# Optimization experiments

Hardware: AMD Instinct MI355X
Metric: run time of the kernel (lower is better)

Reference implementation:

```python
import jax, jax.numpy as jnp
import numpy as np

N, C_IN, C_OUT, J = 4096, 256, 256, 2
ATT_SLICE = C_OUT * J  # 512
DENSITY = 0.01
NEG_FILL = -1e20


def _sparse_lap(key, n):
    k1, k2 = jax.random.split(key)
    vals = jax.random.normal(k1, (n, n), dtype=jnp.float32)
    mask = jax.random.uniform(k2, (n, n)) < DENSITY
    return vals * mask + jnp.eye(n, dtype=jnp.float32)


def setup_inputs() -> dict:
    key = jax.random.key(0)
    ks = jax.random.split(key, 12)
    s = 0.05
    return {
        "x": jax.random.normal(ks[0], (N, C_IN), dtype=jnp.float32),
        "Lup": _sparse_lap(ks[1], N),
        "Ld": _sparse_lap(ks[2], N),
        "P": _sparse_lap(ks[3], N),
        "Wirr_w": jax.random.normal(ks[4], (J, C_OUT, C_IN), dtype=jnp.float32) * s,
        "Wirr_b": jax.random.normal(ks[5], (J, C_OUT), dtype=jnp.float32) * s,
        "Wsol_w": jax.random.normal(ks[6], (J, C_OUT, C_IN), dtype=jnp.float32) * s,
        "Wsol_b": jax.random.normal(ks[7], (J, C_OUT), dtype=jnp.float32) * s,
        "Whar_w": jax.random.normal(ks[8], (C_OUT, C_IN), dtype=jnp.float32) * s,
        "Whar_b": jax.random.normal(ks[9], (C_OUT,), dtype=jnp.float32) * s,
        "att_irr": jax.random.normal(ks[10], (2 * ATT_SLICE, 1), dtype=jnp.float32) * s,
        "att_sol": jax.random.normal(ks[11], (2 * ATT_SLICE, 1), dtype=jnp.float32) * s,
    }


def _branch(x, L, Ww, Wb, att):
    # x_cat = concat_j(Linear_j(x)) : [N, J*C_OUT]
    x_cat = (jnp.einsum('nc,jdc->njd', x, Ww) + Wb).reshape(x.shape[0], -1)
    src = x_cat @ att[:ATT_SLICE, :]   # [N,1]
    dst = x_cat @ att[ATT_SLICE:, :]   # [N,1]
    E = jax.nn.leaky_relu(src + dst.T, negative_slope=0.01)  # [N,N]
    E = jnp.where(L != 0, E, NEG_FILL)
    alpha = jax.nn.softmax(E, axis=-1)
    z = (alpha @ x) @ Ww[0].T + Wb[0]
    for p in range(1, J):  # Laplacian-power diffusion
        alpha = alpha @ L
        z = z + (alpha @ x) @ Ww[p].T + Wb[p]
    return z


def reference(x, Lup, Ld, P, Wirr_w, Wirr_b, Wsol_w, Wsol_b, Whar_w, Whar_b, att_irr, att_sol):
    z_i = _branch(x, Ld, Wirr_w, Wirr_b, att_irr)
    z_s = _branch(x, Lup, Wsol_w, Wsol_b, att_sol)
    z_har = (P @ x) @ Whar_w.T + Whar_b
    return z_i + z_s + z_har
```

## Files before the change

kernel.cpp:

```cpp
#include <hip/hip_runtime.h>

#define NROW 4096
#define CH   256
#define MAXNNZ 128

typedef short  short8  __attribute__((ext_vector_type(8)));
typedef unsigned short ushort8 __attribute__((ext_vector_type(8)));
typedef float  f32x4   __attribute__((ext_vector_type(4)));

__device__ inline unsigned short f2bf(float f) {
  unsigned u = __float_as_uint(f);
  return (unsigned short)((u + 0x7fffu + ((u >> 16) & 1u)) >> 16);
}
__device__ inline float bf2f(unsigned short h) {
  return __uint_as_float((unsigned)h << 16);
}
__device__ inline int mbcnt64(unsigned long long m, int base) {
  int t = __builtin_amdgcn_mbcnt_lo((unsigned)m, (unsigned)base);
  return __builtin_amdgcn_mbcnt_hi((unsigned)(m >> 32), t);
}

__global__ __launch_bounds__(256, 4) void build_csr3(
    const float* __restrict__ L0, const float* __restrict__ L1,
    const float* __restrict__ L2, int* __restrict__ idx,
    float* __restrict__ val, int* __restrict__ cnt) {
  __shared__ int   sj[4][MAXNNZ];
  __shared__ float sv[4][MAXNNZ];
  const int mat = blockIdx.y;
  const float* L = (mat == 0) ? L0 : (mat == 1) ? L1 : L2;
  const int wi = threadIdx.x >> 6, lane = threadIdx.x & 63;
  const int row = blockIdx.x * 4 + wi;
  const float4* Lrow = (const float4*)(L + (size_t)row * NROW);

  float4 v0  = Lrow[lane],        v1  = Lrow[64 + lane];
  float4 v2  = Lrow[128 + lane],  v3  = Lrow[192 + lane];
  float4 v4  = Lrow[256 + lane],  v5  = Lrow[320 + lane];
  float4 v6  = Lrow[384 + lane],  v7  = Lrow[448 + lane];
  float4 v8  = Lrow[512 + lane],  v9  = Lrow[576 + lane];
  float4 v10 = Lrow[640 + lane],  v11 = Lrow[704 + lane];
  float4 v12 = Lrow[768 + lane],  v13 = Lrow[832 + lane];
  float4 v14 = Lrow[896 + lane],  v15 = Lrow[960 + lane];
  __builtin_amdgcn_sched_barrier(0);

  int base = 0;
#define PROCQ(q, cb) {                                                         \
    bool a0 = q.x != 0.f, a1 = q.y != 0.f, a2 = q.z != 0.f, a3 = q.w != 0.f;   \
    unsigned long long b0 = __ballot(a0), b1 = __ballot(a1);                   \
    unsigned long long b2 = __ballot(a2), b3 = __ballot(a3);                   \
    int off = mbcnt64(b3, mbcnt64(b2, mbcnt64(b1, mbcnt64(b0, base))));        \
    if (a0) { if (off < MAXNNZ) { sj[wi][off] = (cb);     sv[wi][off] = q.x; } ++off; } \
    if (a1) { if (off < MAXNNZ) { sj[wi][off] = (cb) + 1; sv[wi][off] = q.y; } ++off; } \
    if (a2) { if (off < MAXNNZ) { sj[wi][off] = (cb) + 2; sv[wi][off] = q.z; } ++off; } \
    if (a3) { if (off < MAXNNZ) { sj[wi][off] = (cb) + 3; sv[wi][off] = q.w; } ++off; } \
    base += __popcll(b0) + __popcll(b1) + __popcll(b2) + __popcll(b3); }
  int cb = lane * 4;
  PROCQ(v0,  cb)        PROCQ(v1,  cb + 256)  PROCQ(v2,  cb + 512)  PROCQ(v3,  cb + 768)
  PROCQ(v4,  cb + 1024) PROCQ(v5,  cb + 1280) PROCQ(v6,  cb + 1536) PROCQ(v7,  cb + 1792)
  PROCQ(v8,  cb + 2048) PROCQ(v9,  cb + 2304) PROCQ(v10, cb + 2560) PROCQ(v11, cb + 2816)
  PROCQ(v12, cb + 3072) PROCQ(v13, cb + 3328) PROCQ(v14, cb + 3584) PROCQ(v15, cb + 3840)
#undef PROCQ

  size_t rbase = ((size_t)mat * NROW + row) * MAXNNZ;
  int2   ji = ((const int2*)sj[wi])[lane];
  float2 vf = ((const float2*)sv[wi])[lane];
  ((int2*)(idx + rbase))[lane] = ji;
  ((float2*)(val + rbase))[lane] = vf;
  if (lane == 0) cnt[mat * NROW + row] = base < MAXNNZ ? base : MAXNNZ;
}

__global__ void cvt_all(const float* __restrict__ x, const float* __restrict__ Wi,
                        const float* __restrict__ Ws, const float* __restrict__ Wh,
                        unsigned short* __restrict__ xbf, unsigned short* __restrict__ Bbf) {
  int i = blockIdx.x * 256 + threadIdx.x;
  const float* src; unsigned short* dst; int o;
  if (i < 262144)        { src = x;  dst = xbf;          o = i; }
  else if (i < 294912)   { src = Wi; dst = Bbf;          o = i - 262144; }
  else if (i < 327680)   { src = Ws; dst = Bbf + 131072; o = i - 294912; }
  else                   { src = Wh; dst = Bbf + 262144; o = i - 327680; }
  float4 v = ((const float4*)src)[o];
  ushort4 u;
  u.x = f2bf(v.x); u.y = f2bf(v.y); u.z = f2bf(v.z); u.w = f2bf(v.w);
  ((ushort4*)dst)[o] = u;
}

__global__ __launch_bounds__(256, 2) void gemm_mfma(const unsigned short* __restrict__ A,
                                                    const unsigned short* __restrict__ Bt,
                                                    unsigned short* __restrict__ Y) {
  __shared__ unsigned short sA[64 * 256];
  __shared__ unsigned short sB[64 * 256];
  const int m0 = blockIdx.x * 64, n0 = blockIdx.y * 64;
  const int tid = threadIdx.x, wid = tid >> 6, lane = tid & 63;

  for (int c = 0; c < 8; ++c) {
    int chunk = c * 256 + tid;
    int r  = chunk >> 5;
    int cb = (chunk & 31) * 16;
    int cbs = cb ^ ((r & 7) << 4);
    ushort8 va = *(const ushort8*)((const char*)(A  + (size_t)(m0 + r) * 256) + cb);
    *(ushort8*)((char*)sA + r * 512 + cbs) = va;
    ushort8 vb = *(const ushort8*)((const char*)(Bt + (size_t)(n0 + r) * 256) + cb);
    *(ushort8*)((char*)sB + r * 512 + cbs) = vb;
  }
  __syncthreads();

  const int wr = wid >> 1, wc = wid & 1;
  const int lr = lane & 15, kg = lane >> 4;
  f32x4 acc[2][2] = {};
#pragma unroll
  for (int ks = 0; ks < 8; ++ks) {
    int kb = ks * 64 + kg * 16;
    short8 a0, a1, b0, b1;
    { int r = wr * 32 + lr;      a0 = *(const short8*)((const char*)sA + r * 512 + (kb ^ ((r & 7) << 4))); }
    { int r = wr * 32 + 16 + lr; a1 = *(const short8*)((const char*)sA + r * 512 + (kb ^ ((r & 7) << 4))); }
    { int r = wc * 32 + lr;      b0 = *(const short8*)((const char*)sB + r * 512 + (kb ^ ((r & 7) << 4))); }
    { int r = wc * 32 + 16 + lr; b1 = *(const short8*)((const char*)sB + r * 512 + (kb ^ ((r & 7) << 4))); }
    acc[0][0] = __builtin_amdgcn_mfma_f32_16x16x32_bf16(a0, b0, acc[0][0], 0, 0, 0);
    acc[0][1] = __builtin_amdgcn_mfma_f32_16x16x32_bf16(a0, b1, acc[0][1], 0, 0, 0);
    acc[1][0] = __builtin_amdgcn_mfma_f32_16x16x32_bf16(a1, b0, acc[1][0], 0, 0, 0);
    acc[1][1] = __builtin_amdgcn_mfma_f32_16x16x32_bf16(a1, b1, acc[1][1], 0, 0, 0);
  }

#pragma unroll
  for (int mi = 0; mi < 2; ++mi)
#pragma unroll
    for (int ni = 0; ni < 2; ++ni) {
      int col = n0 + wc * 32 + ni * 16 + lr;
#pragma unroll
      for (int r4 = 0; r4 < 4; ++r4) {
        int row = m0 + wr * 32 + mi * 16 + kg * 4 + r4;
        Y[(size_t)row * 1280 + col] = f2bf(acc[mi][ni][r4]);
      }
    }
}

__global__ __launch_bounds__(256) void sdv_from_y(
    const unsigned short* __restrict__ Y, const float* __restrict__ ai,
    const float* __restrict__ as_, const float* __restrict__ bi,
    const float* __restrict__ bs, float* __restrict__ sdv) {
  __shared__ float satt[2048];
  __shared__ float sbias[4];
  int t = threadIdx.x, wi = t >> 6, lane = t & 63;
  for (int k = t; k < 1024; k += 256) { satt[k] = ai[k]; satt[1024 + k] = as_[k]; }
  {
    const float* av = (wi & 2) ? as_ : ai;
    const float* bv = (wi & 2) ? bs : bi;
    int off = (wi & 1) * 512;
    float b = 0.f;
    for (int k = lane; k < 512; k += 64) b += av[off + k] * bv[k];
    for (int o = 32; o; o >>= 1) b += __shfl_xor(b, o);
    if (lane == 0) sbias[wi] = b;
  }
  __syncthreads();

  int row = blockIdx.x * 4 + wi;
  const ushort8* yr = (const ushort8*)(Y + (size_t)row * 1280);
  ushort8 ya = yr[lane * 2], yb = yr[lane * 2 + 1];
  int c0 = lane * 16;
  int off = (lane < 32) ? 0 : 512;
  float a0 = 0.f, a1 = 0.f;
#pragma unroll
  for (int j = 0; j < 8; ++j) {
    float y = bf2f(ya[j]); int c = c0 + j;
    a0 += satt[off + c] * y; a1 += satt[off + 512 + c] * y;
  }
#pragma unroll
  for (int j = 0; j < 8; ++j) {
    float y = bf2f(yb[j]); int c = c0 + 8 + j;
    a0 += satt[off + c] * y; a1 += satt[off + 512 + c] * y;
  }
  for (int o = 16; o; o >>= 1) { a0 += __shfl_xor(a0, o); a1 += __shfl_xor(a1, o); }
  if (lane == 0)  { sdv[row] = a0 + sbias[0];            sdv[NROW + row] = a1 + sbias[1]; }
  if (lane == 32) { sdv[2 * NROW + row] = a0 + sbias[2]; sdv[3 * NROW + row] = a1 + sbias[3]; }
}

__global__ __launch_bounds__(256) void spmm_add(const int* __restrict__ idx,
                                                const float* __restrict__ val,
                                                const int* __restrict__ cnt,
                                                unsigned short* __restrict__ Y) {
  int br = blockIdx.y, row = blockIdx.x;
  int t = threadIdx.x, w = t >> 6, l = t & 63;
  __shared__ int   sj[MAXNNZ];
  __shared__ float sv[MAXNNZ];
  __shared__ float part[4][256];
  size_t rbase = ((size_t)br * NROW + row) * MAXNNZ;
  int n = cnt[br * NROW + row];
  if (t < n) { sj[t] = idx[rbase + t]; sv[t] = val[rbase + t]; }
  __syncthreads();
  int cs = br ? 768 : 256, cd = br ? 512 : 0;
  float4 acc = {0.f, 0.f, 0.f, 0.f};
  for (int k = w; k < n; k += 4) {
    ushort4 y = *(const ushort4*)(Y + (size_t)sj[k] * 1280 + cs + 4 * l);
    float a = sv[k];
    acc.x += a * bf2f(y.x); acc.y += a * bf2f(y.y);
    acc.z += a * bf2f(y.z); acc.w += a * bf2f(y.w);
  }
  ((float4*)part[w])[l] = acc;
  __syncthreads();
  if (t < 64) {
    unsigned short* yp = Y + (size_t)row * 1280 + cd + 4 * t;
    ushort4 yb = *(const ushort4*)yp;
    ushort4 o;
    o.x = f2bf(bf2f(yb.x) + part[0][4 * t]     + part[1][4 * t]     + part[2][4 * t]     + part[3][4 * t]);
    o.y = f2bf(bf2f(yb.y) + part[0][4 * t + 1] + part[1][4 * t + 1] + part[2][4 * t + 1] + part[3][4 * t + 1]);
    o.z = f2bf(bf2f(yb.z) + part[0][4 * t + 2] + part[1][4 * t + 2] + part[2][4 * t + 2] + part[3][4 * t + 2]);
    o.w = f2bf(bf2f(yb.w) + part[0][4 * t + 3] + part[1][4 * t + 3] + part[2][4 * t + 3] + part[3][4 * t + 3]);
    *(ushort4*)yp = o;
  }
}

__global__ __launch_bounds__(256) void final_z(const int* __restrict__ idx,
                        const float* __restrict__ val, const int* __restrict__ cnt,
                        const float* __restrict__ sdv,
                        const unsigned short* __restrict__ Y,
                        const float* __restrict__ bi, const float* __restrict__ bs,
                        const float* __restrict__ bh, float* __restrict__ Z) {
  int row = blockIdx.x, t = threadIdx.x, w = t >> 6, l = t & 63;
  __shared__ float sa[MAXNNZ];
  __shared__ int   sj[MAXNNZ];
  __shared__ float red[4];
  __shared__ float part[4][256];
  float4 acc = {0.f, 0.f, 0.f, 0.f};

  for (int br = 0; br < 2; ++br) {
    size_t rbase = ((size_t)br * NROW + row) * MAXNNZ;
    int n = cnt[br * NROW + row];
    const float* srcv = sdv + (2 * br) * NROW;
    const float* dstv = sdv + (2 * br + 1) * NROW;
    float e = -1e30f;
    if (t < n) {
      int j = idx[rbase + t];
      sj[t] = j;
      float v = srcv[row] + dstv[j];
      e = v >= 0.f ? v : 0.01f * v;
    }
    float m = e;
    for (int o = 32; o; o >>= 1) m = fmaxf(m, __shfl_xor(m, o));
    if ((t & 63) == 0) red[t >> 6] = m;
    __syncthreads();
    m = fmaxf(fmaxf(red[0], red[1]), fmaxf(red[2], red[3]));
    __syncthreads();
    float p = (t < n) ? expf(e - m) : 0.f;
    float s = p;
    for (int o = 32; o; o >>= 1) s += __shfl_xor(s, o);
    if ((t & 63) == 0) red[t >> 6] = s;
    __syncthreads();
    s = red[0] + red[1] + red[2] + red[3];
    if (t < n) sa[t] = p / s;
    __syncthreads();
    int cd = br ? 512 : 0;
    for (int k = w; k < n; k += 4) {
      ushort4 y = *(const ushort4*)(Y + (size_t)sj[k] * 1280 + cd + 4 * l);
      float a = sa[k];
      acc.x += a * bf2f(y.x); acc.y += a * bf2f(y.y);
      acc.z += a * bf2f(y.z); acc.w += a * bf2f(y.w);
    }
    __syncthreads();
  }

  {
    size_t rbase = ((size_t)2 * NROW + row) * MAXNNZ;
    int n = cnt[2 * NROW + row];
    if (t < n) { sj[t] = idx[rbase + t]; sa[t] = val[rbase + t]; }
    __syncthreads();
    for (int k = w; k < n; k += 4) {
      ushort4 y = *(const ushort4*)(Y + (size_t)sj[k] * 1280 + 1024 + 4 * l);
      float a = sa[k];
      acc.x += a * bf2f(y.x); acc.y += a * bf2f(y.y);
      acc.z += a * bf2f(y.z); acc.w += a * bf2f(y.w);
    }
  }
  ((float4*)part[w])[l] = acc;
  __syncthreads();
  if (t < 64) {
    float4 r;
    int c = 4 * t;
    r.x = part[0][c]     + part[1][c]     + part[2][c]     + part[3][c]     + bi[c]     + bi[256 + c]     + bs[c]     + bs[256 + c]     + bh[c];
    r.y = part[0][c + 1] + part[1][c + 1] + part[2][c + 1] + part[3][c + 1] + bi[c + 1] + bi[257 + c]     + bs[c + 1] + bs[257 + c]     + bh[c + 1];
    r.z = part[0][c + 2] + part[1][c + 2] + part[2][c + 2] + part[3][c + 2] + bi[c + 2] + bi[258 + c]     + bs[c + 2] + bs[258 + c]     + bh[c + 2];
    r.w = part[0][c + 3] + part[1][c + 3] + part[2][c + 3] + part[3][c + 3] + bi[c + 3] + bi[259 + c]     + bs[c + 3] + bs[259 + c]     + bh[c + 3];
    *(float4*)(Z + (size_t)row * 256 + c) = r;
  }
}

extern "C" void kernel_launch(void* const* d_in, const int* in_sizes, int n_in,
                              void* d_out, int out_size, void* d_ws, size_t ws_size,
                              hipStream_t stream) {
  const float* x      = (const float*)d_in[0];
  const float* Lup    = (const float*)d_in[1];
  const float* Ld     = (const float*)d_in[2];
  const float* P      = (const float*)d_in[3];
  const float* Wirr_w = (const float*)d_in[4];
  const float* Wirr_b = (const float*)d_in[5];
  const float* Wsol_w = (const float*)d_in[6];
  const float* Wsol_b = (const float*)d_in[7];
  const float* Whar_w = (const float*)d_in[8];
  const float* Whar_b = (const float*)d_in[9];
  const float* att_i  = (const float*)d_in[10];
  const float* att_s  = (const float*)d_in[11];
  float* Z = (float*)d_out;

  char* w = (char*)d_ws;
  auto alloc = [&](size_t bytes) { void* p = (void*)w; w += (bytes + 255) & ~(size_t)255; return p; };

  int*   idx  = (int*)alloc((size_t)3 * NROW * MAXNNZ * 4);
  float* val  = (float*)alloc((size_t)3 * NROW * MAXNNZ * 4);
  int*   cnt  = (int*)alloc((size_t)3 * NROW * 4);
  float* sdv  = (float*)alloc(4 * NROW * 4);
  unsigned short* xbf = (unsigned short*)alloc((size_t)NROW * CH * 2);
  unsigned short* Bbf = (unsigned short*)alloc((size_t)1280 * CH * 2);
  unsigned short* Y   = (unsigned short*)alloc((size_t)NROW * 1280 * 2);

  build_csr3<<<dim3(NROW / 4, 3), 256, 0, stream>>>(Ld, Lup, P, idx, val, cnt);

  cvt_all<<<(262144 + 32768 + 32768 + 16384) / 256, 256, 0, stream>>>(x, Wirr_w, Wsol_w, Whar_w, xbf, Bbf);

  gemm_mfma<<<dim3(NROW / 64, 1280 / 64), 256, 0, stream>>>(xbf, Bbf, Y);

  sdv_from_y<<<NROW / 4, 256, 0, stream>>>(Y, att_i, att_s, Wirr_b, Wsol_b, sdv);

  spmm_add<<<dim3(NROW, 2), 256, 0, stream>>>(idx, val, cnt, Y);

  final_z<<<NROW, 256, 0, stream>>>(idx, val, cnt, sdv, Y, Wirr_b, Wsol_b, Whar_b, Z);
}
```

Measured before the change: 114.1 us.

## Fuse CSR scan with GEMM via interleaved blocks and merge sdv into spmm

The dense-to-CSR scan and the MFMA projection GEMM now run in one launch. Every tenth block does a GEMM tile in two K-halves with a smaller shared buffer, and the rest scan one row each, split across four waves. The separate sdv and spmm kernels are merged into a single per-row kernel that computes both attention dot products and both branch SpMMs. The aim is fewer launches and letting the GEMM work overlap the bandwidth-bound scan of the three dense matrices. In exchange the scan now uses one block per row instead of four rows per block, and the merged row kernel adds extra barriers and shared memory.

Measured after the change: 107.8 us. 1.06x faster.

```diff
diff --git a/kernel.cpp b/kernel.cpp
--- a/kernel.cpp
+++ b/kernel.cpp
@@ -18,54 +18,6 @@
 __device__ inline int mbcnt64(unsigned long long m, int base) {
   int t = __builtin_amdgcn_mbcnt_lo((unsigned)m, (unsigned)base);
   return __builtin_amdgcn_mbcnt_hi((unsigned)(m >> 32), t);
-}
-
-__global__ __launch_bounds__(256, 4) void build_csr3(
-    const float* __restrict__ L0, const float* __restrict__ L1,
-    const float* __restrict__ L2, int* __restrict__ idx,
-    float* __restrict__ val, int* __restrict__ cnt) {
-  __shared__ int   sj[4][MAXNNZ];
-  __shared__ float sv[4][MAXNNZ];
-  const int mat = blockIdx.y;
-  const float* L = (mat == 0) ? L0 : (mat == 1) ? L1 : L2;
-  const int wi = threadIdx.x >> 6, lane = threadIdx.x & 63;
-  const int row = blockIdx.x * 4 + wi;
-  const float4* Lrow = (const float4*)(L + (size_t)row * NROW);
-
-  float4 v0  = Lrow[lane],        v1  = Lrow[64 + lane];
-  float4 v2  = Lrow[128 + lane],  v3  = Lrow[192 + lane];
-  float4 v4  = Lrow[256 + lane],  v5  = Lrow[320 + lane];
-  float4 v6  = Lrow[384 + lane],  v7  = Lrow[448 + lane];
-  float4 v8  = Lrow[512 + lane],  v9  = Lrow[576 + lane];
-  float4 v10 = Lrow[640 + lane],  v11 = Lrow[704 + lane];
-  float4 v12 = Lrow[768 + lane],  v13 = Lrow[832 + lane];
-  float4 v14 = Lrow[896 + lane],  v15 = Lrow[960 + lane];
-  __builtin_amdgcn_sched_barrier(0);
-
-  int base = 0;
-#define PROCQ(q, cb) {                                                         \
-    bool a0 = q.x != 0.f, a1 = q.y != 0.f, a2 = q.z != 0.f, a3 = q.w != 0.f;   \
-    unsigned long long b0 = __ballot(a0), b1 = __ballot(a1);                   \
-    unsigned long long b2 = __ballot(a2), b3 = __ballot(a3);                   \
-    int off = mbcnt64(b3, mbcnt64(b2, mbcnt64(b1, mbcnt64(b0, base))));        \
-    if (a0) { if (off < MAXNNZ) { sj[wi][off] = (cb);     sv[wi][off] = q.x; } ++off; } \
-    if (a1) { if (off < MAXNNZ) { sj[wi][off] = (cb) + 1; sv[wi][off] = q.y; } ++off; } \
-    if (a2) { if (off < MAXNNZ) { sj[wi][off] = (cb) + 2; sv[wi][off] = q.z; } ++off; } \
-    if (a3) { if (off < MAXNNZ) { sj[wi][off] = (cb) + 3; sv[wi][off] = q.w; } ++off; } \
-    base += __popcll(b0) + __popcll(b1) + __popcll(b2) + __popcll(b3); }
-  int cb = lane * 4;
-  PROCQ(v0,  cb)        PROCQ(v1,  cb + 256)  PROCQ(v2,  cb + 512)  PROCQ(v3,  cb + 768)
-  PROCQ(v4,  cb + 1024) PROCQ(v5,  cb + 1280) PROCQ(v6,  cb + 1536) PROCQ(v7,  cb + 1792)
-  PROCQ(v8,  cb + 2048) PROCQ(v9,  cb + 2304) PROCQ(v10, cb + 2560) PROCQ(v11, cb + 2816)
-  PROCQ(v12, cb + 3072) PROCQ(v13, cb + 3328) PROCQ(v14, cb + 3584) PROCQ(v15, cb + 3840)
-#undef PROCQ
-
-  size_t rbase = ((size_t)mat * NROW + row) * MAXNNZ;
-  int2   ji = ((const int2*)sj[wi])[lane];
-  float2 vf = ((const float2*)sv[wi])[lane];
-  ((int2*)(idx + rbase))[lane] = ji;
-  ((float2*)(val + rbase))[lane] = vf;
-  if (lane == 0) cnt[mat * NROW + row] = base < MAXNNZ ? base : MAXNNZ;
 }
 
 __global__ void cvt_all(const float* __restrict__ x, const float* __restrict__ Wi,
@@ -83,121 +35,188 @@
   ((ushort4*)dst)[o] = u;
 }
 
-__global__ __launch_bounds__(256, 2) void gemm_mfma(const unsigned short* __restrict__ A,
-                                                    const unsigned short* __restrict__ Bt,
-                                                    unsigned short* __restrict__ Y) {
-  __shared__ unsigned short sA[64 * 256];
-  __shared__ unsigned short sB[64 * 256];
-  const int m0 = blockIdx.x * 64, n0 = blockIdx.y * 64;
-  const int tid = threadIdx.x, wid = tid >> 6, lane = tid & 63;
-
-  for (int c = 0; c < 8; ++c) {
-    int chunk = c * 256 + tid;
-    int r  = chunk >> 5;
-    int cb = (chunk & 31) * 16;
-    int cbs = cb ^ ((r & 7) << 4);
-    ushort8 va = *(const ushort8*)((const char*)(A  + (size_t)(m0 + r) * 256) + cb);
-    *(ushort8*)((char*)sA + r * 512 + cbs) = va;
-    ushort8 vb = *(const ushort8*)((const char*)(Bt + (size_t)(n0 + r) * 256) + cb);
-    *(ushort8*)((char*)sB + r * 512 + cbs) = vb;
-  }
-  __syncthreads();
-
-  const int wr = wid >> 1, wc = wid & 1;
-  const int lr = lane & 15, kg = lane >> 4;
-  f32x4 acc[2][2] = {};
-#pragma unroll
-  for (int ks = 0; ks < 8; ++ks) {
-    int kb = ks * 64 + kg * 16;
-    short8 a0, a1, b0, b1;
-    { int r = wr * 32 + lr;      a0 = *(const short8*)((const char*)sA + r * 512 + (kb ^ ((r & 7) << 4))); }
-    { int r = wr * 32 + 16 + lr; a1 = *(const short8*)((const char*)sA + r * 512 + (kb ^ ((r & 7) << 4))); }
-    { int r = wc * 32 + lr;      b0 = *(const short8*)((const char*)sB + r * 512 + (kb ^ ((r & 7) << 4))); }
-    { int r = wc * 32 + 16 + lr; b1 = *(const short8*)((const char*)sB + r * 512 + (kb ^ ((r & 7) << 4))); }
-    acc[0][0] = __builtin_amdgcn_mfma_f32_16x16x32_bf16(a0, b0, acc[0][0], 0, 0, 0);
-    acc[0][1] = __builtin_amdgcn_mfma_f32_16x16x32_bf16(a0, b1, acc[0][1], 0, 0, 0);
-    acc[1][0] = __builtin_amdgcn_mfma_f32_16x16x32_bf16(a1, b0, acc[1][0], 0, 0, 0);
-    acc[1][1] = __builtin_amdgcn_mfma_f32_16x16x32_bf16(a1, b1, acc[1][1], 0, 0, 0);
-  }
-
-#pragma unroll
-  for (int mi = 0; mi < 2; ++mi)
-#pragma unroll
-    for (int ni = 0; ni < 2; ++ni) {
-      int col = n0 + wc * 32 + ni * 16 + lr;
-#pragma unroll
-      for (int r4 = 0; r4 < 4; ++r4) {
-        int row = m0 + wr * 32 + mi * 16 + kg * 4 + r4;
-        Y[(size_t)row * 1280 + col] = f2bf(acc[mi][ni][r4]);
+__global__ __launch_bounds__(256) void scan_gemm(
+    const float* __restrict__ L0, const float* __restrict__ L1,
+    const float* __restrict__ L2, int* __restrict__ idx,
+    float* __restrict__ val, int* __restrict__ cnt,
+    const unsigned short* __restrict__ A, const unsigned short* __restrict__ Bt,
+    unsigned short* __restrict__ Y) {
+  __shared__ __align__(16) union {
+    struct { unsigned short sA[64 * 128]; unsigned short sB[64 * 128]; } g;
+    struct { int sj[4][MAXNNZ]; float sv[4][MAXNNZ]; int scnt[4]; } c;
+  } u;
+  const int bid = blockIdx.x, tid = threadIdx.x;
+  const bool is_gemm = (bid < 12800) && (bid % 10 == 9);
+
+  if (is_gemm) {
+    const int gid = bid / 10;
+    const int m0 = (gid & 63) * 64, n0 = (gid >> 6) * 64;
+    const int wid = tid >> 6, lane = tid & 63;
+    const int wr = wid >> 1, wc = wid & 1, lr = lane & 15, kg = lane >> 4;
+    f32x4 acc[2][2] = {};
+#pragma unroll
+    for (int kh = 0; kh < 2; ++kh) {
+      for (int c = 0; c < 4; ++c) {
+        int chunk = c * 256 + tid;
+        int r  = chunk >> 4;
+        int cb = (chunk & 15) * 16;
+        int cbs = cb ^ ((r & 7) << 4);
+        ushort8 va = *(const ushort8*)((const char*)A  + (size_t)(m0 + r) * 512 + kh * 256 + cb);
+        *(ushort8*)((char*)u.g.sA + r * 256 + cbs) = va;
+        ushort8 vb = *(const ushort8*)((const char*)Bt + (size_t)(n0 + r) * 512 + kh * 256 + cb);
+        *(ushort8*)((char*)u.g.sB + r * 256 + cbs) = vb;
       }
-    }
-}
-
-__global__ __launch_bounds__(256) void sdv_from_y(
-    const unsigned short* __restrict__ Y, const float* __restrict__ ai,
+      __syncthreads();
+#pragma unroll
+      for (int ks = 0; ks < 4; ++ks) {
+        int kb = ks * 64 + kg * 16;
+        short8 a0, a1, b0, b1;
+        { int r = wr * 32 + lr;      a0 = *(const short8*)((const char*)u.g.sA + r * 256 + (kb ^ ((r & 7) << 4))); }
+        { int r = wr * 32 + 16 + lr; a1 = *(const short8*)((const char*)u.g.sA + r * 256 + (kb ^ ((r & 7) << 4))); }
+        { int r = wc * 32 + lr;      b0 = *(const short8*)((const char*)u.g.sB + r * 256 + (kb ^ ((r & 7) << 4))); }
+        { int r = wc * 32 + 16 + lr; b1 = *(const short8*)((const char*)u.g.sB + r * 256 + (kb ^ ((r & 7) << 4))); }
+        acc[0][0] = __builtin_amdgcn_mfma_f32_16x16x32_bf16(a0, b0, acc[0][0], 0, 0, 0);
+        acc[0][1] = __builtin_amdgcn_mfma_f32_16x16x32_bf16(a0, b1, acc[0][1], 0, 0, 0);
+        acc[1][0] = __builtin_amdgcn_mfma_f32_16x16x32_bf16(a1, b0, acc[1][0], 0, 0, 0);
+        acc[1][1] = __builtin_amdgcn_mfma_f32_16x16x32_bf16(a1, b1, acc[1][1], 0, 0, 0);
+      }
+      __syncthreads();
+    }
+#pragma unroll
+    for (int mi = 0; mi < 2; ++mi)
+#pragma unroll
+      for (int ni = 0; ni < 2; ++ni) {
+        int col = n0 + wc * 32 + ni * 16 + lr;
+#pragma unroll
+        for (int r4 = 0; r4 < 4; ++r4) {
+          int row = m0 + wr * 32 + mi * 16 + kg * 4 + r4;
+          Y[(size_t)row * 1280 + col] = f2bf(acc[mi][ni][r4]);
+        }
+      }
+  } else {
+    const int cid = bid - ((bid < 12800) ? (bid + 1) / 10 : 1280);
+    const int mat = cid >> 12, row = cid & 4095;
+    const float* L = (mat == 0) ? L0 : (mat == 1) ? L1 : L2;
+    const int wi = tid >> 6, lane = tid & 63;
+    const float4* Lseg = (const float4*)(L + (size_t)row * NROW) + wi * 256;
+
+    float4 v0 = Lseg[lane], v1 = Lseg[64 + lane], v2 = Lseg[128 + lane], v3 = Lseg[192 + lane];
+
+    int base = 0;
+    float4 vv[4] = {v0, v1, v2, v3};
+#pragma unroll
+    for (int k = 0; k < 4; ++k) {
+      float4 q = vv[k];
+      bool n0_ = q.x != 0.f, n1_ = q.y != 0.f, n2_ = q.z != 0.f, n3_ = q.w != 0.f;
+      unsigned long long b0 = __ballot(n0_), b1 = __ballot(n1_);
+      unsigned long long b2 = __ballot(n2_), b3 = __ballot(n3_);
+      int off = mbcnt64(b3, mbcnt64(b2, mbcnt64(b1, mbcnt64(b0, base))));
+      int col0 = wi * 1024 + k * 256 + lane * 4;
+      if (n0_) { if (off < MAXNNZ) { u.c.sj[wi][off] = col0;     u.c.sv[wi][off] = q.x; } ++off; }
+      if (n1_) { if (off < MAXNNZ) { u.c.sj[wi][off] = col0 + 1; u.c.sv[wi][off] = q.y; } ++off; }
+      if (n2_) { if (off < MAXNNZ) { u.c.sj[wi][off] = col0 + 2; u.c.sv[wi][off] = q.z; } ++off; }
+      if (n3_) { if (off < MAXNNZ) { u.c.sj[wi][off] = col0 + 3; u.c.sv[wi][off] = q.w; } ++off; }
+      base += __popcll(b0) + __popcll(b1) + __popcll(b2) + __popcll(b3);
+    }
+    if (lane == 0) u.c.scnt[wi] = base < MAXNNZ ? base : MAXNNZ;
+    __syncthreads();
+
+    int c0 = u.c.scnt[0], c1 = u.c.scnt[1], c2 = u.c.scnt[2], c3 = u.c.scnt[3];
+    int total = c0 + c1 + c2 + c3;
+    if (total > MAXNNZ) total = MAXNNZ;
+    size_t rbase = ((size_t)mat * NROW + row) * MAXNNZ;
+    int t = tid;
+    if (t < total) {
+      int s, o;
+      if      (t < c0)           { s = 0; o = t; }
+      else if (t < c0 + c1)      { s = 1; o = t - c0; }
+      else if (t < c0 + c1 + c2) { s = 2; o = t - c0 - c1; }
+      else                       { s = 3; o = t - c0 - c1 - c2; }
+      idx[rbase + t] = u.c.sj[s][o];
+      val[rbase + t] = u.c.sv[s][o];
+    }
+    if (t == 0) cnt[mat * NROW + row] = total;
+  }
+}
+
+__global__ __launch_bounds__(256) void spmm_sdv(
+    const int* __restrict__ idx, const float* __restrict__ val,
+    const int* __restrict__ cnt, const float* __restrict__ ai,
     const float* __restrict__ as_, const float* __restrict__ bi,
-    const float* __restrict__ bs, float* __restrict__ sdv) {
+    const float* __restrict__ bs, unsigned short* __restrict__ Y,
+    float* __restrict__ sdv) {
+  int row = blockIdx.x, t = threadIdx.x, w = t >> 6, l = t & 63;
   __shared__ float satt[2048];
+  __shared__ float red2[8];
   __shared__ float sbias[4];
-  int t = threadIdx.x, wi = t >> 6, lane = t & 63;
+  __shared__ int   sj0[MAXNNZ], sj1[MAXNNZ];
+  __shared__ float sv0[MAXNNZ], sv1[MAXNNZ];
+  __shared__ float part[4][256];
+
   for (int k = t; k < 1024; k += 256) { satt[k] = ai[k]; satt[1024 + k] = as_[k]; }
   {
-    const float* av = (wi & 2) ? as_ : ai;
-    const float* bv = (wi & 2) ? bs : bi;
-    int off = (wi & 1) * 512;
+    const float* av = (w & 2) ? as_ : ai;
+    const float* bv = (w & 2) ? bs : bi;
+    int off = (w & 1) * 512;
     float b = 0.f;
-    for (int k = lane; k < 512; k += 64) b += av[off + k] * bv[k];
+    for (int k = l; k < 512; k += 64) b += av[off + k] * bv[k];
     for (int o = 32; o; o >>= 1) b += __shfl_xor(b, o);
-    if (lane == 0) sbias[wi] = b;
-  }
-  __syncthreads();
-
-  int row = blockIdx.x * 4 + wi;
-  const ushort8* yr = (const ushort8*)(Y + (size_t)row * 1280);
-  ushort8 ya = yr[lane * 2], yb = yr[lane * 2 + 1];
-  int c0 = lane * 16;
-  int off = (lane < 32) ? 0 : 512;
-  float a0 = 0.f, a1 = 0.f;
-#pragma unroll
-  for (int j = 0; j < 8; ++j) {
-    float y = bf2f(ya[j]); int c = c0 + j;
-    a0 += satt[off + c] * y; a1 += satt[off + 512 + c] * y;
-  }
-#pragma unroll
-  for (int j = 0; j < 8; ++j) {
-    float y = bf2f(yb[j]); int c = c0 + 8 + j;
-    a0 += satt[off + c] * y; a1 += satt[off + 512 + c] * y;
-  }
-  for (int o = 16; o; o >>= 1) { a0 += __shfl_xor(a0, o); a1 += __shfl_xor(a1, o); }
-  if (lane == 0)  { sdv[row] = a0 + sbias[0];            sdv[NROW + row] = a1 + sbias[1]; }
-  if (lane == 32) { sdv[2 * NROW + row] = a0 + sbias[2]; sdv[3 * NROW + row] = a1 + sbias[3]; }
-}
-
-__global__ __launch_bounds__(256) void spmm_add(const int* __restrict__ idx,
-                                                const float* __restrict__ val,
-                                                const int* __restrict__ cnt,
-                                                unsigned short* __restrict__ Y) {
-  int br = blockIdx.y, row = blockIdx.x;
-  int t = threadIdx.x, w = t >> 6, l = t & 63;
-  __shared__ int   sj[MAXNNZ];
-  __shared__ float sv[MAXNNZ];
-  __shared__ float part[4][256];
-  size_t rbase = ((size_t)br * NROW + row) * MAXNNZ;
-  int n = cnt[br * NROW + row];
-  if (t < n) { sj[t] = idx[rbase + t]; sv[t] = val[rbase + t]; }
-  __syncthreads();
-  int cs = br ? 768 : 256, cd = br ? 512 : 0;
-  float4 acc = {0.f, 0.f, 0.f, 0.f};
-  for (int k = w; k < n; k += 4) {
-    ushort4 y = *(const ushort4*)(Y + (size_t)sj[k] * 1280 + cs + 4 * l);
-    float a = sv[k];
-    acc.x += a * bf2f(y.x); acc.y += a * bf2f(y.y);
-    acc.z += a * bf2f(y.z); acc.w += a * bf2f(y.w);
-  }
-  ((float4*)part[w])[l] = acc;
-  __syncthreads();
+    if (l == 0) sbias[w] = b;
+  }
+  int n0 = cnt[row], n1 = cnt[NROW + row];
+  if (t < n0) { sj0[t] = idx[(size_t)row * MAXNNZ + t];          sv0[t] = val[(size_t)row * MAXNNZ + t]; }
+  if (t < n1) { sj1[t] = idx[((size_t)NROW + row) * MAXNNZ + t]; sv1[t] = val[((size_t)NROW + row) * MAXNNZ + t]; }
+  ushort4 y4 = *(const ushort4*)(Y + (size_t)row * 1280 + 4 * t);
+  __syncthreads();
+
+  {
+    int c0 = 4 * t;
+    int aoff = (t < 128) ? 0 : 1024;
+    int cc = c0 & 511;
+    float sp = satt[aoff + cc]       * bf2f(y4.x) + satt[aoff + cc + 1]       * bf2f(y4.y)
+             + satt[aoff + cc + 2]   * bf2f(y4.z) + satt[aoff + cc + 3]       * bf2f(y4.w);
+    float dp = satt[aoff + 512 + cc] * bf2f(y4.x) + satt[aoff + 512 + cc + 1] * bf2f(y4.y)
+             + satt[aoff + 512 + cc + 2] * bf2f(y4.z) + satt[aoff + 512 + cc + 3] * bf2f(y4.w);
+    for (int o = 32; o; o >>= 1) { sp += __shfl_xor(sp, o); dp += __shfl_xor(dp, o); }
+    if (l == 0) { red2[w * 2] = sp; red2[w * 2 + 1] = dp; }
+  }
+
+  float4 acc0 = {0.f, 0.f, 0.f, 0.f}, acc1 = {0.f, 0.f, 0.f, 0.f};
+  for (int k = w; k < n0; k += 4) {
+    ushort4 y = *(const ushort4*)(Y + (size_t)sj0[k] * 1280 + 256 + 4 * l);
+    float a = sv0[k];
+    acc0.x += a * bf2f(y.x); acc0.y += a * bf2f(y.y);
+    acc0.z += a * bf2f(y.z); acc0.w += a * bf2f(y.w);
+  }
+  for (int k = w; k < n1; k += 4) {
+    ushort4 y = *(const ushort4*)(Y + (size_t)sj1[k] * 1280 + 768 + 4 * l);
+    float a = sv1[k];
+    acc1.x += a * bf2f(y.x); acc1.y += a * bf2f(y.y);
+    acc1.z += a * bf2f(y.z); acc1.w += a * bf2f(y.w);
+  }
+  ((float4*)part[w])[l] = acc0;
+  __syncthreads();
+  if (t == 0) {
+    sdv[row]            = red2[0] + red2[2] + sbias[0];
+    sdv[NROW + row]     = red2[1] + red2[3] + sbias[1];
+    sdv[2 * NROW + row] = red2[4] + red2[6] + sbias[2];
+    sdv[3 * NROW + row] = red2[5] + red2[7] + sbias[3];
+  }
   if (t < 64) {
-    unsigned short* yp = Y + (size_t)row * 1280 + cd + 4 * t;
+    unsigned short* yp = Y + (size_t)row * 1280 + 4 * t;
+    ushort4 yb = *(const ushort4*)yp;
+    ushort4 o;
+    o.x = f2bf(bf2f(yb.x) + part[0][4 * t]     + part[1][4 * t]     + part[2][4 * t]     + part[3][4 * t]);
+    o.y = f2bf(bf2f(yb.y) + part[0][4 * t + 1] + part[1][4 * t + 1] + part[2][4 * t + 1] + part[3][4 * t + 1]);
+    o.z = f2bf(bf2f(yb.z) + part[0][4 * t + 2] + part[1][4 * t + 2] + part[2][4 * t + 2] + part[3][4 * t + 2]);
+    o.w = f2bf(bf2f(yb.w) + part[0][4 * t + 3] + part[1][4 * t + 3] + part[2][4 * t + 3] + part[3][4 * t + 3]);
+    *(ushort4*)yp = o;
+  }
+  __syncthreads();
+  ((float4*)part[w])[l] = acc1;
+  __syncthreads();
+  if (t < 64) {
+    unsigned short* yp = Y + (size_t)row * 1280 + 512 + 4 * t;
     ushort4 yb = *(const ushort4*)yp;
     ushort4 o;
     o.x = f2bf(bf2f(yb.x) + part[0][4 * t]     + part[1][4 * t]     + part[2][4 * t]     + part[3][4 * t]);
@@ -274,10 +293,10 @@
   if (t < 64) {
     float4 r;
     int c = 4 * t;
-    r.x = part[0][c]     + part[1][c]     + part[2][c]     + part[3][c]     + bi[c]     + bi[256 + c]     + bs[c]     + bs[256 + c]     + bh[c];
-    r.y = part[0][c + 1] + part[1][c + 1] + part[2][c + 1] + part[3][c + 1] + bi[c + 1] + bi[257 + c]     + bs[c + 1] + bs[257 + c]     + bh[c + 1];
-    r.z = part[0][c + 2] + part[1][c + 2] + part[2][c + 2] + part[3][c + 2] + bi[c + 2] + bi[258 + c]     + bs[c + 2] + bs[258 + c]     + bh[c + 2];
-    r.w = part[0][c + 3] + part[1][c + 3] + part[2][c + 3] + part[3][c + 3] + bi[c + 3] + bi[259 + c]     + bs[c + 3] + bs[259 + c]     + bh[c + 3];
+    r.x = part[0][c]     + part[1][c]     + part[2][c]     + part[3][c]     + bi[c]     + bi[256 + c] + bs[c]     + bs[256 + c] + bh[c];
+    r.y = part[0][c + 1] + part[1][c + 1] + part[2][c + 1] + part[3][c + 1] + bi[c + 1] + bi[257 + c] + bs[c + 1] + bs[257 + c] + bh[c + 1];
+    r.z = part[0][c + 2] + part[1][c + 2] + part[2][c + 2] + part[3][c + 2] + bi[c + 2] + bi[258 + c] + bs[c + 2] + bs[258 + c] + bh[c + 2];
+    r.w = part[0][c + 3] + part[1][c + 3] + part[2][c + 3] + part[3][c + 3] + bi[c + 3] + bi[259 + c] + bs[c + 3] + bs[259 + c] + bh[c + 3];
     *(float4*)(Z + (size_t)row * 256 + c) = r;
   }
 }
@@ -310,15 +329,11 @@
   unsigned short* Bbf = (unsigned short*)alloc((size_t)1280 * CH * 2);
   unsigned short* Y   = (unsigned short*)alloc((size_t)NROW * 1280 * 2);
 
-  build_csr3<<<dim3(NROW / 4, 3), 256, 0, stream>>>(Ld, Lup, P, idx, val, cnt);
-
   cvt_all<<<(262144 + 32768 + 32768 + 16384) / 256, 256, 0, stream>>>(x, Wirr_w, Wsol_w, Whar_w, xbf, Bbf);
 
-  gemm_mfma<<<dim3(NROW / 64, 1280 / 64), 256, 0, stream>>>(xbf, Bbf, Y);
-
-  sdv_from_y<<<NROW / 4, 256, 0, stream>>>(Y, att_i, att_s, Wirr_b, Wsol_b, sdv);
-
-  spmm_add<<<dim3(NROW, 2), 256, 0, stream>>>(idx, val, cnt, Y);
+  scan_gemm<<<13568, 256, 0, stream>>>(Ld, Lup, P, idx, val, cnt, xbf, Bbf, Y);
+
+  spmm_sdv<<<NROW, 256, 0, stream>>>(idx, val, cnt, att_i, att_s, Wirr_b, Wsol_b, Y, sdv);
 
   final_z<<<NROW, 256, 0, stream>>>(idx, val, cnt, sdv, Y, Wirr_b, Wsol_b, Whar_b, Z);
 }
```
